# Optimization experiments

Hardware: AMD Instinct MI355X
Metric: run time of the kernel (lower is better)

The kernel has to match this reference:

```python
import jax, jax.numpy as jnp
import numpy as np
from jax.scipy.linalg import solve_triangular

N, K, D = 131072, 8, 32  # samples, clusters, dims


def setup_inputs() -> dict:
    key = jax.random.key(0)
    k1, k2, k3, k4 = jax.random.split(key, 4)
    return {
        "X": jax.random.normal(k1, (N, D), dtype=jnp.float32),
        "mu": jax.random.normal(k2, (K, D), dtype=jnp.float32),
        "L": jax.random.normal(k3, (K, D, D), dtype=jnp.float32),
        "weights": jax.random.normal(k4, (K,), dtype=jnp.float32),
        "it": 0,
    }


def _mixture_log_likelihoods(X, mu, L, weights):
    K_, D_ = mu.shape
    LOG2PI = float(np.log(2.0 * np.pi))
    # update_covariances: A_k = L_k L_k^T + I  (always SPD -> cholesky succeeds)
    A = jnp.einsum('kab,kcb->kac', L, L) + jnp.eye(D_, dtype=L.dtype)
    Lc = jnp.linalg.cholesky(A)            # [K,D,D] lower Cholesky factors
    invLc = jnp.linalg.inv(Lc)             # [K,D,D]
    # all cluster pairs (cartesian_prod order: i outer, j inner)
    ii, jj = [g.reshape(-1) for g in jnp.meshgrid(jnp.arange(K_), jnp.arange(K_), indexing='ij')]
    Si, Sj = Lc[ii], Lc[jj]                # NOTE: original uses the CHOLESKY FACTORS here
    invSi, invSj = invLc[ii], invLc[jj]
    mui, muj = mu[ii], mu[jj]
    # _gaussian_product: sigma = inv(inv(Si)+inv(Sj)); mu = sigma @ (inv(Si) mu_i + inv(Sj) mu_j)
    sigma = jnp.linalg.inv(invSi + invSj)                      # [P,D,D]
    rhs = jnp.einsum('pab,pb->pa', invSi, mui) + jnp.einsum('pab,pb->pa', invSj, muj)
    mu_p = jnp.einsum('pab,pb->pa', sigma, rhs)                # [P,D]
    # _product_z: log(1/sqrt(det(2*pi*(Si+Sj))) * exp(-0.5 dmu^T inv(Si+Sj) dmu))
    S = Si + Sj
    dmu = mui - muj
    quad = -0.5 * jnp.einsum('pa,pab,pb->p', dmu, jnp.linalg.inv(S), dmu)
    z = -0.5 * jnp.log(jnp.linalg.det(2.0 * np.pi * S)) + quad  # [P]
    # _unormalised_pdf: lower-triangular solve against sigma (only lower triangle used)
    diff = X[None, :, :] - mu_p[:, None, :]                    # [P,N,D]
    m = solve_triangular(sigma, jnp.swapaxes(diff, 1, 2), lower=True)  # [P,D,N]
    ll = -0.5 * (jnp.sum(m * m, axis=1) + D_ * LOG2PI
                 + jnp.log(jnp.linalg.det(sigma))[:, None])    # [P,N]
    logw = jax.nn.log_softmax(weights)                         # softmax weights, then log
    logprob = z[:, None] + ll + logw[ii][:, None] + logw[jj][:, None]  # [P,N]
    return jnp.log(jnp.sum(jnp.exp(logprob), axis=0))          # [N]


def reference(X, mu, L, weights, it):
    ll = _mixture_log_likelihoods(X, mu, L, weights)
    return jax.scipy.special.logsumexp(ll, axis=0)  # scalar
```

## Files before the change

### kernel.cpp

```cpp
#include <hip/hip_runtime.h>

#define D 32
#define K 8
#define NPAIR 36

#define MOFF 0
#define WOFF 8192
#define C2OFF 8448
#define CMAXOFF 8484
#define LCOFF 8512
#define PARTOFF 16704

typedef float v2f __attribute__((ext_vector_type(2)));

__host__ __device__ constexpr int gidx(int i, int j) {
    return i * 8 + j - i * (i + 1) / 2;
}

__global__ __launch_bounds__(64) void setup1_kernel(
    const float* __restrict__ mu, const float* __restrict__ L,
    float* __restrict__ ws)
{
    __shared__ float sA[D][D + 1];
    __shared__ float sLc[D][D + 1];
    const int k = blockIdx.x;
    const int tid = threadIdx.x;
    const int i = tid & 31;

    const float* Lk = L + k * D * D;
    for (int e = tid; e < D * D; e += 64) {
        const int a = e >> 5, c = e & 31;
        float s = (a == c) ? 1.0f : 0.0f;
        #pragma unroll
        for (int b = 0; b < D; ++b) s = fmaf(Lk[a * D + b], Lk[c * D + b], s);
        sA[a][c] = s;
    }
    __syncthreads();

    float lrow[D];
    #pragma unroll
    for (int j = 0; j < D; ++j) {
        if (i == j) {
            float s = sA[j][j];
            #pragma unroll
            for (int b = 0; b < j; ++b) s = fmaf(-lrow[b], lrow[b], s);
            const float d = sqrtf(s);
            lrow[j] = d;
            #pragma unroll
            for (int b = 0; b < j; ++b) sLc[j][b] = lrow[b];
            sLc[j][j] = d;
        }
        __syncthreads();
        if (i > j) {
            float s = sA[i][j];
            #pragma unroll
            for (int b = 0; b < j; ++b) s = fmaf(-lrow[b], sLc[j][b], s);
            lrow[j] = s / sLc[j][j];
        }
    }
    __syncthreads();

    #pragma unroll
    for (int b = 0; b < D; ++b)
        ws[LCOFF + k * D * D + i * D + b] = (b <= i) ? lrow[b] : 0.0f;

    {
        const int j = i;
        float col[D];
        #pragma unroll
        for (int ii = 0; ii < D; ++ii) {
            float s = (ii == j) ? 1.0f : 0.0f;
            #pragma unroll
            for (int b = 0; b < ii; ++b) {
                const float m = (b >= j) ? sLc[ii][b] : 0.0f;
                s = fmaf(-m, col[b], s);
            }
            col[ii] = s / sLc[ii][ii];
            ws[MOFF + k * D * D + ii * D + j] = col[ii];
        }
        #pragma unroll
        for (int ii = 0; ii < D; ++ii) sA[ii][j] = col[ii];
    }
    __syncthreads();

    {
        float s = 0.0f;
        #pragma unroll
        for (int b = 0; b < D; ++b) s = fmaf(sA[i][b], mu[k * D + b], s);
        ws[WOFF + k * D + i] = s;
    }
}

#define SLC(kk, r, c) sLc2[(kk) * 1024 + (r) * 32 + (c)]

__global__ __launch_bounds__(64) void setup2_kernel(
    const float* __restrict__ mu, const float* __restrict__ weights,
    float* __restrict__ ws)
{
    __shared__ float sLc2[K * D * D];
    __shared__ float sLogw[K];
    __shared__ float sCp[NPAIR];
    __shared__ float sCmax;
    const int tid = threadIdx.x;

    {
        const float4* src = (const float4*)(ws + LCOFF);
        float4* dst = (float4*)sLc2;
        for (int e = tid; e < K * D * D / 4; e += 64) dst[e] = src[e];
    }
    if (tid == 0) {
        float m = -INFINITY;
        for (int t = 0; t < K; ++t) m = fmaxf(m, weights[t]);
        float s = 0.0f;
        for (int t = 0; t < K; ++t) s += expf(weights[t] - m);
        const float lse = m + logf(s);
        for (int t = 0; t < K; ++t) sLogw[t] = weights[t] - lse;
    }
    __syncthreads();

    if (tid < NPAIR) {
        int tt = tid, pi = 0;
        while (tt >= (K - pi)) { tt -= (K - pi); ++pi; }
        const int pj = pi + tt;
        const float LOG2PI = 1.8378770664093453f;
        float sumlogS = 0.0f, logdetsig = 0.0f;
        #pragma unroll
        for (int r = 0; r < D; ++r) {
            const float di = SLC(pi, r, r), dj = SLC(pj, r, r);
            sumlogS += logf(di + dj);
            logdetsig -= logf(1.0f / di + 1.0f / dj);
        }
        float v[D];
        float quad_acc = 0.0f;
        #pragma unroll
        for (int r = 0; r < D; ++r) {
            const float d0 = mu[pi * D + r] - mu[pj * D + r];
            float s = d0;
            #pragma unroll
            for (int b = 0; b < r; ++b)
                s = fmaf(-(SLC(pi, r, b) + SLC(pj, r, b)), v[b], s);
            v[r] = s / (SLC(pi, r, r) + SLC(pj, r, r));
            quad_acc = fmaf(d0, v[r], quad_acc);
        }
        const float quad = -0.5f * quad_acc;
        float c = quad - 0.5f * sumlogS - (float)D * LOG2PI - 0.5f * logdetsig
                  + sLogw[pi] + sLogw[pj];
        if (pi < pj) c += 0.6931471805599453f;
        sCp[tid] = c;
    }
    __syncthreads();
    if (tid == 0) {
        float m = -INFINITY;
        for (int t = 0; t < NPAIR; ++t) m = fmaxf(m, sCp[t]);
        sCmax = m;
        ws[CMAXOFF] = m;
    }
    __syncthreads();
    if (tid < NPAIR)
        ws[C2OFF + tid] = (sCp[tid] - sCmax) * 1.4426950408889634f;
}

__global__ __launch_bounds__(128, 1) void main_kernel(
    const float* __restrict__ X, const float* __restrict__ cst,
    float* __restrict__ partials, int nsamp)
{
    __shared__ __align__(16) float sM[K * D * D];
    __shared__ float sW[K * D];
    __shared__ float sC2[NPAIR];
    __shared__ float sRed[2];
    const int tid = threadIdx.x;

    {
        const float4* src = (const float4*)cst;
        float4* dst = (float4*)sM;
        for (int e = tid; e < K * D * D / 4; e += 128) dst[e] = src[e];
        for (int e = tid; e < K * D; e += 128) sW[e] = cst[WOFF + e];
        if (tid < NPAIR) sC2[tid] = cst[C2OFF + tid];
    }
    __syncthreads();

    const int n0 = blockIdx.x * 256 + tid;
    const int n1 = n0 + 128;
    const bool val0 = n0 < nsamp, val1 = n1 < nsamp;
    const int m0 = val0 ? n0 : 0, m1 = val1 ? n1 : 0;

    v2f x0[16], x1[16];
    {
        const float4* Xv0 = (const float4*)(X + m0 * D);
        const float4* Xv1 = (const float4*)(X + m1 * D);
        #pragma unroll
        for (int q = 0; q < 8; ++q) {
            const float4 t0 = Xv0[q];
            x0[2 * q] = (v2f){t0.x, t0.y}; x0[2 * q + 1] = (v2f){t0.z, t0.w};
            const float4 t1 = Xv1[q];
            x1[2 * q] = (v2f){t1.x, t1.y}; x1[2 * q + 1] = (v2f){t1.z, t1.w};
        }
    }

    v2f G2[NPAIR];
    #pragma unroll
    for (int t = 0; t < NPAIR; ++t) G2[t] = (v2f){0.0f, 0.0f};

    #pragma unroll
    for (int rh = 0; rh < 8; ++rh) {
        v2f yp[K][4];
        #pragma unroll
        for (int k = 0; k < K; ++k) {
            #pragma unroll
            for (int rr = 0; rr < 4; ++rr) {
                const int r = 4 * rh + rr;
                const float wv = sW[k * D + r];
                v2f a0 = (v2f){-wv, 0.0f};
                v2f a1 = (v2f){-wv, 0.0f};
                const float* Mr = sM + (k * D + r) * D;
                #pragma unroll
                for (int c4 = 0; c4 <= rh; ++c4) {
                    const float4 m4 = *(const float4*)(Mr + 4 * c4);
                    const v2f mlo = (v2f){m4.x, m4.y};
                    const v2f mhi = (v2f){m4.z, m4.w};
                    a0 = __builtin_elementwise_fma(mlo, x0[2 * c4], a0);
                    a0 = __builtin_elementwise_fma(mhi, x0[2 * c4 + 1], a0);
                    a1 = __builtin_elementwise_fma(mlo, x1[2 * c4], a1);
                    a1 = __builtin_elementwise_fma(mhi, x1[2 * c4 + 1], a1);
                }
                yp[k][rr] = (v2f){a0.x + a0.y, a1.x + a1.y};
            }
        }
        #pragma unroll
        for (int pi = 0; pi < K; ++pi)
            #pragma unroll
            for (int pj = pi; pj < K; ++pj) {
                v2f g = G2[gidx(pi, pj)];
                g = __builtin_elementwise_fma(yp[pi][0], yp[pj][0], g);
                g = __builtin_elementwise_fma(yp[pi][1], yp[pj][1], g);
                g = __builtin_elementwise_fma(yp[pi][2], yp[pj][2], g);
                g = __builtin_elementwise_fma(yp[pi][3], yp[pj][3], g);
                G2[gidx(pi, pj)] = g;
            }
    }

    v2f acc2 = (v2f){0.0f, 0.0f};
    const float NH = -0.72134752044448170f;
    #pragma unroll
    for (int pi = 0; pi < K; ++pi)
        #pragma unroll
        for (int pj = pi; pj < K; ++pj) {
            const v2f q2 = __builtin_elementwise_fma(
                (v2f){2.0f, 2.0f}, G2[gidx(pi, pj)],
                G2[gidx(pi, pi)] + G2[gidx(pj, pj)]);
            const float c = sC2[gidx(pi, pj)];
            const v2f e2 = __builtin_elementwise_fma((v2f){NH, NH}, q2, (v2f){c, c});
            acc2.x += exp2f(e2.x);
            acc2.y += exp2f(e2.y);
        }
    float acc = (val0 ? acc2.x : 0.0f) + (val1 ? acc2.y : 0.0f);

    #pragma unroll
    for (int m = 1; m < 64; m <<= 1) acc += __shfl_xor(acc, m, 64);
    if ((tid & 63) == 0) sRed[tid >> 6] = acc;
    __syncthreads();
    if (tid == 0) partials[blockIdx.x] = sRed[0] + sRed[1];
}

__global__ __launch_bounds__(256) void finish_kernel(
    const float* __restrict__ partials, const float* __restrict__ ws,
    float* __restrict__ out, int nblk)
{
    __shared__ float sRed[4];
    const int tid = threadIdx.x;
    float acc = 0.0f;
    for (int e = tid; e < nblk; e += 256) acc += partials[e];
    #pragma unroll
    for (int m = 1; m < 64; m <<= 1) acc += __shfl_xor(acc, m, 64);
    if ((tid & 63) == 0) sRed[tid >> 6] = acc;
    __syncthreads();
    if (tid == 0) out[0] = ws[CMAXOFF] + logf(sRed[0] + sRed[1] + sRed[2] + sRed[3]);
}

extern "C" void kernel_launch(void* const* d_in, const int* in_sizes, int n_in,
                              void* d_out, int out_size, void* d_ws, size_t ws_size,
                              hipStream_t stream) {
    const float* X = (const float*)d_in[0];
    const float* mu = (const float*)d_in[1];
    const float* L = (const float*)d_in[2];
    const float* w = (const float*)d_in[3];
    float* wsf = (float*)d_ws;
    float* out = (float*)d_out;

    const int nsamp = in_sizes[0] / D;
    const int nblk = (nsamp + 255) / 256;

    setup1_kernel<<<K, 64, 0, stream>>>(mu, L, wsf);
    setup2_kernel<<<1, 64, 0, stream>>>(mu, w, wsf);
    main_kernel<<<nblk, 128, 0, stream>>>(X, wsf, wsf + PARTOFF, nsamp);
    finish_kernel<<<1, 256, 0, stream>>>(wsf + PARTOFF, wsf, out, nblk);
}
```

Before: 158.1 us.

## Pack triangular inverse factors, one sample per thread, two blocks per CU

The triangular inverse factors are now stored in a packed lower-triangular layout (rounded up to 4-wide groups), so the staged constant data shrinks by about half. The main kernel processes one sample per thread instead of two, with packed row-pairs in the Gram accumulation, and launch bounds now allow two blocks per CU. Setup1 is rewritten to do the Cholesky with wave shuffles instead of per-column barriers. The aim is to cut register pressure and LDS footprint to raise occupancy, at the cost of less per-thread reuse of LDS matrix loads across samples.

Result: faster. 153.9 us (-2.6%).

```diff
diff --git a/kernel.cpp b/kernel.cpp
--- a/kernel.cpp
+++ b/kernel.cpp
@@ -3,92 +3,97 @@
 #define D 32
 #define K 8
 #define NPAIR 36
-
-#define MOFF 0
-#define WOFF 8192
-#define C2OFF 8448
-#define CMAXOFF 8484
-#define LCOFF 8512
-#define PARTOFF 16704
+#define PROWS 576
+
+#define PMOFF 0
+#define WOFF 4608
+#define C2OFF 4864
+#define CMAXOFF 4900
+#define STAGE_F4 1226
+#define LCOFF 4928
+#define PARTOFF 13120
 
 typedef float v2f __attribute__((ext_vector_type(2)));
 
 __host__ __device__ constexpr int gidx(int i, int j) {
     return i * 8 + j - i * (i + 1) / 2;
+}
+__host__ __device__ constexpr int proff(int r) {
+    return 4 * (r / 4 + 1) * (2 * (r / 4) + (r % 4));
 }
 
 __global__ __launch_bounds__(64) void setup1_kernel(
     const float* __restrict__ mu, const float* __restrict__ L,
     float* __restrict__ ws)
 {
-    __shared__ float sA[D][D + 1];
-    __shared__ float sLc[D][D + 1];
+    __shared__ float sL[D][D + 1];
+    __shared__ float sI[D][D + 1];
     const int k = blockIdx.x;
     const int tid = threadIdx.x;
     const int i = tid & 31;
 
-    const float* Lk = L + k * D * D;
-    for (int e = tid; e < D * D; e += 64) {
-        const int a = e >> 5, c = e & 31;
-        float s = (a == c) ? 1.0f : 0.0f;
-        #pragma unroll
-        for (int b = 0; b < D; ++b) s = fmaf(Lk[a * D + b], Lk[c * D + b], s);
-        sA[a][c] = s;
-    }
-    __syncthreads();
-
-    float lrow[D];
+    for (int e = tid; e < D * D; e += 64) sL[e >> 5][e & 31] = L[k * D * D + e];
+    __syncthreads();
+
+    float l[D];
+    #pragma unroll
+    for (int b = 0; b < D; ++b) l[b] = sL[i][b];
+
+    float a[D];
+    #pragma unroll
+    for (int c = 0; c < D; ++c) {
+        float s = (i == c) ? 1.0f : 0.0f;
+        #pragma unroll
+        for (int b = 0; b < D; ++b) s = fmaf(l[b], sL[c][b], s);
+        a[c] = s;
+    }
+
+    float lc[D];
     #pragma unroll
     for (int j = 0; j < D; ++j) {
-        if (i == j) {
-            float s = sA[j][j];
-            #pragma unroll
-            for (int b = 0; b < j; ++b) s = fmaf(-lrow[b], lrow[b], s);
-            const float d = sqrtf(s);
-            lrow[j] = d;
-            #pragma unroll
-            for (int b = 0; b < j; ++b) sLc[j][b] = lrow[b];
-            sLc[j][j] = d;
-        }
-        __syncthreads();
-        if (i > j) {
-            float s = sA[i][j];
-            #pragma unroll
-            for (int b = 0; b < j; ++b) s = fmaf(-lrow[b], sLc[j][b], s);
-            lrow[j] = s / sLc[j][j];
-        }
-    }
-    __syncthreads();
-
-    #pragma unroll
-    for (int b = 0; b < D; ++b)
-        ws[LCOFF + k * D * D + i * D + b] = (b <= i) ? lrow[b] : 0.0f;
-
-    {
-        const int j = i;
-        float col[D];
-        #pragma unroll
-        for (int ii = 0; ii < D; ++ii) {
-            float s = (ii == j) ? 1.0f : 0.0f;
-            #pragma unroll
-            for (int b = 0; b < ii; ++b) {
-                const float m = (b >= j) ? sLc[ii][b] : 0.0f;
-                s = fmaf(-m, col[b], s);
-            }
-            col[ii] = s / sLc[ii][ii];
-            ws[MOFF + k * D * D + ii * D + j] = col[ii];
-        }
-        #pragma unroll
-        for (int ii = 0; ii < D; ++ii) sA[ii][j] = col[ii];
-    }
-    __syncthreads();
-
-    {
+        const float pivot = __shfl(a[j], j, 64);
+        const float dinv = 1.0f / sqrtf(pivot);
+        const float lij = a[j] * dinv;
+        lc[j] = lij;
+        #pragma unroll
+        for (int c = j + 1; c < D; ++c)
+            a[c] = fmaf(-lij, __shfl(lij, c, 64), a[c]);
+    }
+
+    __syncthreads();
+    #pragma unroll
+    for (int b = 0; b < D; ++b) sL[i][b] = (b <= i) ? lc[b] : 0.0f;
+    __syncthreads();
+
+    float col[D];
+    #pragma unroll
+    for (int ii = 0; ii < D; ++ii) {
+        float s = (ii == i) ? 1.0f : 0.0f;
+        #pragma unroll
+        for (int b = 0; b < ii; ++b) s = fmaf(-sL[ii][b], col[b], s);
+        col[ii] = s / sL[ii][ii];
+    }
+
+    #pragma unroll
+    for (int ii = 0; ii < D; ++ii) {
+        const int w4 = 4 * (ii / 4 + 1);
+        if (i < w4) ws[PMOFF + k * PROWS + proff(ii) + i] = col[ii];
+    }
+
+    #pragma unroll
+    for (int ii = 0; ii < D; ++ii) sI[ii][i] = col[ii];
+    __syncthreads();
+
+    {
+        const float mv = mu[k * D + i];
         float s = 0.0f;
         #pragma unroll
-        for (int b = 0; b < D; ++b) s = fmaf(sA[i][b], mu[k * D + b], s);
+        for (int b = 0; b < D; ++b) s = fmaf(sI[i][b], __shfl(mv, b, 64), s);
         ws[WOFF + k * D + i] = s;
     }
+
+    for (int e = tid; e < D * D; e += 64)
+        ws[LCOFF + k * D * D + e] = sL[e >> 5][e & 31];
 }
 
 #define SLC(kk, r, c) sLc2[(kk) * 1024 + (r) * 32 + (c)]
@@ -160,42 +165,34 @@
         ws[C2OFF + tid] = (sCp[tid] - sCmax) * 1.4426950408889634f;
 }
 
-__global__ __launch_bounds__(128, 1) void main_kernel(
+__global__ __launch_bounds__(128, 2) void main_kernel(
     const float* __restrict__ X, const float* __restrict__ cst,
     float* __restrict__ partials, int nsamp)
 {
-    __shared__ __align__(16) float sM[K * D * D];
-    __shared__ float sW[K * D];
-    __shared__ float sC2[NPAIR];
+    __shared__ __align__(16) float sAll[STAGE_F4 * 4];
     __shared__ float sRed[2];
     const int tid = threadIdx.x;
+    const int n = blockIdx.x * 128 + tid;
+    const bool valid = n < nsamp;
+    const int m = valid ? n : 0;
+
+    v2f x[16];
+    {
+        const float4* Xv = (const float4*)(X + m * D);
+        #pragma unroll
+        for (int q = 0; q < 8; ++q) {
+            const float4 t = Xv[q];
+            x[2 * q] = (v2f){t.x, t.y};
+            x[2 * q + 1] = (v2f){t.z, t.w};
+        }
+    }
 
     {
         const float4* src = (const float4*)cst;
-        float4* dst = (float4*)sM;
-        for (int e = tid; e < K * D * D / 4; e += 128) dst[e] = src[e];
-        for (int e = tid; e < K * D; e += 128) sW[e] = cst[WOFF + e];
-        if (tid < NPAIR) sC2[tid] = cst[C2OFF + tid];
-    }
-    __syncthreads();
-
-    const int n0 = blockIdx.x * 256 + tid;
-    const int n1 = n0 + 128;
-    const bool val0 = n0 < nsamp, val1 = n1 < nsamp;
-    const int m0 = val0 ? n0 : 0, m1 = val1 ? n1 : 0;
-
-    v2f x0[16], x1[16];
-    {
-        const float4* Xv0 = (const float4*)(X + m0 * D);
-        const float4* Xv1 = (const float4*)(X + m1 * D);
-        #pragma unroll
-        for (int q = 0; q < 8; ++q) {
-            const float4 t0 = Xv0[q];
-            x0[2 * q] = (v2f){t0.x, t0.y}; x0[2 * q + 1] = (v2f){t0.z, t0.w};
-            const float4 t1 = Xv1[q];
-            x1[2 * q] = (v2f){t1.x, t1.y}; x1[2 * q + 1] = (v2f){t1.z, t1.w};
-        }
-    }
+        float4* dst = (float4*)sAll;
+        for (int e = tid; e < STAGE_F4; e += 128) dst[e] = src[e];
+    }
+    __syncthreads();
 
     v2f G2[NPAIR];
     #pragma unroll
@@ -203,27 +200,25 @@
 
     #pragma unroll
     for (int rh = 0; rh < 8; ++rh) {
-        v2f yp[K][4];
+        v2f yp[K][2];
         #pragma unroll
         for (int k = 0; k < K; ++k) {
+            const float* base = sAll + k * PROWS;
             #pragma unroll
             for (int rr = 0; rr < 4; ++rr) {
                 const int r = 4 * rh + rr;
-                const float wv = sW[k * D + r];
-                v2f a0 = (v2f){-wv, 0.0f};
-                v2f a1 = (v2f){-wv, 0.0f};
-                const float* Mr = sM + (k * D + r) * D;
+                const float wv = sAll[WOFF + k * D + r];
+                v2f a = (v2f){-wv, 0.0f};
+                const float* Mr = base + proff(r);
                 #pragma unroll
                 for (int c4 = 0; c4 <= rh; ++c4) {
                     const float4 m4 = *(const float4*)(Mr + 4 * c4);
-                    const v2f mlo = (v2f){m4.x, m4.y};
-                    const v2f mhi = (v2f){m4.z, m4.w};
-                    a0 = __builtin_elementwise_fma(mlo, x0[2 * c4], a0);
-                    a0 = __builtin_elementwise_fma(mhi, x0[2 * c4 + 1], a0);
-                    a1 = __builtin_elementwise_fma(mlo, x1[2 * c4], a1);
-                    a1 = __builtin_elementwise_fma(mhi, x1[2 * c4 + 1], a1);
+                    a = __builtin_elementwise_fma((v2f){m4.x, m4.y}, x[2 * c4], a);
+                    a = __builtin_elementwise_fma((v2f){m4.z, m4.w}, x[2 * c4 + 1], a);
                 }
-                yp[k][rr] = (v2f){a0.x + a0.y, a1.x + a1.y};
+                const float yr = a.x + a.y;
+                if (rr & 1) yp[k][rr >> 1].y = yr;
+                else        yp[k][rr >> 1].x = yr;
             }
         }
         #pragma unroll
@@ -233,30 +228,27 @@
                 v2f g = G2[gidx(pi, pj)];
                 g = __builtin_elementwise_fma(yp[pi][0], yp[pj][0], g);
                 g = __builtin_elementwise_fma(yp[pi][1], yp[pj][1], g);
-                g = __builtin_elementwise_fma(yp[pi][2], yp[pj][2], g);
-                g = __builtin_elementwise_fma(yp[pi][3], yp[pj][3], g);
                 G2[gidx(pi, pj)] = g;
             }
     }
 
-    v2f acc2 = (v2f){0.0f, 0.0f};
+    float G[NPAIR];
+    #pragma unroll
+    for (int t = 0; t < NPAIR; ++t) G[t] = G2[t].x + G2[t].y;
+
+    float acc = 0.0f;
     const float NH = -0.72134752044448170f;
     #pragma unroll
     for (int pi = 0; pi < K; ++pi)
         #pragma unroll
         for (int pj = pi; pj < K; ++pj) {
-            const v2f q2 = __builtin_elementwise_fma(
-                (v2f){2.0f, 2.0f}, G2[gidx(pi, pj)],
-                G2[gidx(pi, pi)] + G2[gidx(pj, pj)]);
-            const float c = sC2[gidx(pi, pj)];
-            const v2f e2 = __builtin_elementwise_fma((v2f){NH, NH}, q2, (v2f){c, c});
-            acc2.x += exp2f(e2.x);
-            acc2.y += exp2f(e2.y);
-        }
-    float acc = (val0 ? acc2.x : 0.0f) + (val1 ? acc2.y : 0.0f);
-
-    #pragma unroll
-    for (int m = 1; m < 64; m <<= 1) acc += __shfl_xor(acc, m, 64);
+            const float q = fmaf(2.0f, G[gidx(pi, pj)], G[gidx(pi, pi)] + G[gidx(pj, pj)]);
+            acc += exp2f(fmaf(NH, q, sAll[C2OFF + gidx(pi, pj)]));
+        }
+    if (!valid) acc = 0.0f;
+
+    #pragma unroll
+    for (int s = 1; s < 64; s <<= 1) acc += __shfl_xor(acc, s, 64);
     if ((tid & 63) == 0) sRed[tid >> 6] = acc;
     __syncthreads();
     if (tid == 0) partials[blockIdx.x] = sRed[0] + sRed[1];
@@ -271,7 +263,7 @@
     float acc = 0.0f;
     for (int e = tid; e < nblk; e += 256) acc += partials[e];
     #pragma unroll
-    for (int m = 1; m < 64; m <<= 1) acc += __shfl_xor(acc, m, 64);
+    for (int s = 1; s < 64; s <<= 1) acc += __shfl_xor(acc, s, 64);
     if ((tid & 63) == 0) sRed[tid >> 6] = acc;
     __syncthreads();
     if (tid == 0) out[0] = ws[CMAXOFF] + logf(sRed[0] + sRed[1] + sRed[2] + sRed[3]);
@@ -288,7 +280,7 @@
     float* out = (float*)d_out;
 
     const int nsamp = in_sizes[0] / D;
-    const int nblk = (nsamp + 255) / 256;
+    const int nblk = (nsamp + 127) / 128;
 
     setup1_kernel<<<K, 64, 0, stream>>>(mu, L, wsf);
     setup2_kernel<<<1, 64, 0, stream>>>(mu, w, wsf);
```
